# Kernel optimization log

Measured on AMD Instinct MI355X. Metric: run time of the kernel, lower is better.

The kernel has to match this reference:

```python
import jax, jax.numpy as jnp
import numpy as np

NUM_GRAPHS = 128

def gcn_conv(x, edge_index, W, b):
    # PyG GCNConv: add self-loops, sym-normalize, aggregate.
    n = x.shape[0]
    src, dst = edge_index[0], edge_index[1]
    h = x @ W                                   # [N, H]
    deg = jnp.zeros((n,), h.dtype).at[dst].add(1.0) + 1.0  # +1 for self-loop
    dinv = jax.lax.rsqrt(deg)                   # deg^-1/2
    norm = dinv[src] * dinv[dst]                # [E]
    msg = h[src] * norm[:, None]                # [E, H] gathered messages
    agg = jnp.zeros_like(h).at[dst].add(msg)    # scatter-add to dst
    agg = agg + h * (dinv * dinv)[:, None]      # self-loop term
    return agg + b


def setup_inputs() -> dict:
    key = jax.random.key(0)
    ks = jax.random.split(key, 12)
    N, E, F, H, C = 50000, 800000, 64, 64, 16
    x = jax.random.normal(ks[0], (N, F), jnp.float32)
    edge_index = jax.random.randint(ks[1], (2, E), 0, N, jnp.int64)
    batch = jnp.sort(jax.random.randint(ks[2], (N,), 0, NUM_GRAPHS, jnp.int64))
    s = lambda k, sh: jax.random.normal(k, sh, jnp.float32) * (1.0 / np.sqrt(sh[0]))
    return {
        "x": x, "edge_index": edge_index, "batch": batch,
        "W1": s(ks[3], (F, H)), "b1": jnp.zeros((H,), jnp.float32),
        "W2": s(ks[4], (H, H)), "b2": jnp.zeros((H,), jnp.float32),
        "Wc1": s(ks[5], (H, H)), "bc1": jnp.zeros((H,), jnp.float32),
        "Wc2": s(ks[6], (H, C)), "bc2": jnp.zeros((C,), jnp.float32),
    }


def reference(x, edge_index, batch, W1, b1, W2, b2, Wc1, bc1, Wc2, bc2):
    h = gcn_conv(x, edge_index, W1, b1)
    h = jax.nn.relu(h)
    # F.dropout(p=0.5, training=self.training): identity in eval mode
    h = gcn_conv(h, edge_index, W2, b2)
    # global mean pool over graphs
    sums = jax.ops.segment_sum(h, batch, num_segments=NUM_GRAPHS)
    cnts = jax.ops.segment_sum(jnp.ones((h.shape[0],), h.dtype), batch,
                               num_segments=NUM_GRAPHS)
    graph_reps = sums / jnp.maximum(cnts, 1.0)[:, None]
    logits = jax.nn.relu(graph_reps @ Wc1 + bc1) @ Wc2 + bc2
    return (h, graph_reps, logits)
```

## Files before the change

### kernel.cpp

```cpp
#include <hip/hip_runtime.h>
#include <hip/hip_bf16.h>

typedef __hip_bfloat16 bf16;

#define NGRAPH 128
#define MAXNB 256
#define BCAP 8192

__global__ __launch_bounds__(256) void bucket_count_kernel(const int* __restrict__ ei,
                                                           int* __restrict__ bucket_cnt,
                                                           int E, int N, int nb) {
    __shared__ int hist[MAXNB];
    for (int i = threadIdx.x; i < nb; i += 256) hist[i] = 0;
    __syncthreads();
    int stride = gridDim.x * 256;
    for (int e = blockIdx.x * 256 + threadIdx.x; e < E; e += stride) {
        int d = ei[E + e];
        d = max(0, min(d, N - 1));
        atomicAdd(&hist[d >> 8], 1);
    }
    __syncthreads();
    for (int i = threadIdx.x; i < nb; i += 256) {
        int c = hist[i];
        if (c) atomicAdd(&bucket_cnt[i], c);
    }
}

__global__ __launch_bounds__(256) void bucket_scan_kernel(const int* __restrict__ bucket_cnt,
                                                          int* __restrict__ bucket_off,
                                                          int* __restrict__ bucket_cur, int nb) {
    __shared__ int tmp[256];
    int tid = threadIdx.x;
    int v = (tid < nb) ? bucket_cnt[tid] : 0;
    tmp[tid] = v;
    __syncthreads();
    for (int off = 1; off < 256; off <<= 1) {
        int t = (tid >= off) ? tmp[tid - off] : 0;
        __syncthreads();
        tmp[tid] += t;
        __syncthreads();
    }
    int excl = tmp[tid] - v;
    if (tid < nb) { bucket_off[tid] = excl; bucket_cur[tid] = excl; }
    if (tid == nb - 1) bucket_off[nb] = excl + v;
}

__global__ __launch_bounds__(256) void bucket_scatter_kernel(const int* __restrict__ ei,
                                                             int* __restrict__ bucket_cur,
                                                             int* __restrict__ pairbuf,
                                                             int E, int N, int nb) {
    __shared__ int hist[MAXNB];
    int nwg = gridDim.x;
    int chunk = (E + nwg - 1) / nwg;
    int e0 = blockIdx.x * chunk;
    int e1 = e0 + chunk; if (e1 > E) e1 = E;
    if (e0 >= e1) return;
    for (int i = threadIdx.x; i < nb; i += 256) hist[i] = 0;
    __syncthreads();
    for (int e = e0 + threadIdx.x; e < e1; e += 256) {
        int d = ei[E + e];
        d = max(0, min(d, N - 1));
        atomicAdd(&hist[d >> 8], 1);
    }
    __syncthreads();
    for (int i = threadIdx.x; i < nb; i += 256) {
        int c = hist[i];
        hist[i] = c ? atomicAdd(&bucket_cur[i], c) : 0;
    }
    __syncthreads();
    for (int e = e0 + threadIdx.x; e < e1; e += 256) {
        int s = ei[e];     s = max(0, min(s, N - 1));
        int d = ei[E + e]; d = max(0, min(d, N - 1));
        int pos = atomicAdd(&hist[d >> 8], 1);
        pairbuf[pos] = (s << 8) | (d & 255);
    }
}

__global__ __launch_bounds__(256) void bucket_build_kernel(const int* __restrict__ pairbuf,
                                                           const int* __restrict__ bucket_off,
                                                           int* __restrict__ row_start,
                                                           float* __restrict__ dinv,
                                                           int* __restrict__ csr_src,
                                                           int E, int N, int nb) {
    __shared__ int deg_l[256];
    __shared__ int cur_l[256];
    __shared__ int stage[BCAP];
    int b = blockIdx.x;
    int node0 = b << 8;
    int nn = N - node0; if (nn > 256) nn = 256;
    int p0 = bucket_off[b], p1 = bucket_off[b + 1];
    int ne = p1 - p0;
    int tid = threadIdx.x;
    deg_l[tid] = 0;
    __syncthreads();
    for (int i = p0 + tid; i < p1; i += 256) {
        int dl = pairbuf[i] & 255;
        atomicAdd(&deg_l[dl], 1);
    }
    __syncthreads();
    int v = deg_l[tid];
    for (int off = 1; off < 256; off <<= 1) {
        int t = (tid >= off) ? deg_l[tid - off] : 0;
        __syncthreads();
        deg_l[tid] += t;
        __syncthreads();
    }
    int excl = deg_l[tid] - v;
    if (tid < nn) {
        row_start[node0 + tid] = p0 + excl;
        dinv[node0 + tid] = rsqrtf((float)(v + 1));
    }
    if (b == nb - 1 && tid == nn - 1) row_start[N] = p0 + excl + v;
    cur_l[tid] = excl;
    __syncthreads();
    if (ne <= BCAP) {
        for (int i = p0 + tid; i < p1; i += 256) {
            int pr = pairbuf[i];
            int pos = atomicAdd(&cur_l[pr & 255], 1);
            stage[pos] = pr >> 8;
        }
        __syncthreads();
        for (int i = tid; i < ne; i += 256) csr_src[p0 + i] = stage[i];
    } else {
        for (int i = p0 + tid; i < p1; i += 256) {
            int pr = pairbuf[i];
            int pos = atomicAdd(&cur_l[pr & 255], 1);
            csr_src[p0 + pos] = pr >> 8;
        }
    }
}

__global__ __launch_bounds__(256) void proj_kernel(const float* __restrict__ A,
                                                   const float* __restrict__ W,
                                                   const float* __restrict__ dinv,
                                                   bf16* __restrict__ P, int N) {
    __shared__ float Wl[4096];
    for (int i = threadIdx.x; i < 4096; i += 256) Wl[i] = W[i];
    __syncthreads();
    int lane = threadIdx.x & 63;
    int wid = (blockIdx.x * 256 + threadIdx.x) >> 6;
    int nwaves = (gridDim.x * 256) >> 6;
    for (int node = wid; node < N; node += nwaves) {
        float a = A[(size_t)node * 64 + lane];
        float acc = 0.f;
#pragma unroll
        for (int k = 0; k < 64; ++k) acc += __shfl(a, k) * Wl[k * 64 + lane];
        P[(size_t)node * 64 + lane] = __float2bfloat16(acc * dinv[node]);
    }
}

__device__ __forceinline__ void acc_bf8(float* acc, uint4 v, float w) {
    unsigned int u[4] = {v.x, v.y, v.z, v.w};
#pragma unroll
    for (int m = 0; m < 4; ++m) {
        float lo = __uint_as_float(u[m] << 16);
        float hi = __uint_as_float(u[m] & 0xffff0000u);
        acc[2 * m]     += w * lo;
        acc[2 * m + 1] += w * hi;
    }
}

__device__ __forceinline__ void gather_sum8(float* acc,
                                            const bf16* __restrict__ P,
                                            const int* __restrict__ csr_src,
                                            int beg, int end, int r, int c) {
#pragma unroll
    for (int k = 0; k < 8; ++k) acc[k] = 0.f;
    for (int i = beg; i < end; i += 16) {
        int r0 = i + r, r1 = i + 8 + r;
        int ok0 = (r0 < end), ok1 = (r1 < end);
        int s0 = ok0 ? csr_src[r0] : 0;
        int s1 = ok1 ? csr_src[r1] : 0;
        float w0 = ok0 ? 1.f : 0.f;
        float w1 = ok1 ? 1.f : 0.f;
        uint4 v0 = *(const uint4*)(P + (size_t)s0 * 64 + c * 8);
        uint4 v1 = *(const uint4*)(P + (size_t)s1 * 64 + c * 8);
        acc_bf8(acc, v0, w0);
        acc_bf8(acc, v1, w1);
    }
#pragma unroll
    for (int mask = 8; mask <= 32; mask <<= 1) {
#pragma unroll
        for (int k = 0; k < 8; ++k) acc[k] += __shfl_xor(acc[k], mask);
    }
}

__global__ __launch_bounds__(256) void agg_proj_kernel(const bf16* __restrict__ P1,
                                                       const int* __restrict__ row_start,
                                                       const int* __restrict__ csr_src,
                                                       const float* __restrict__ dinv,
                                                       const float* __restrict__ b1,
                                                       const float* __restrict__ W2,
                                                       bf16* __restrict__ P2, int N) {
    __shared__ float Wl[4096];
    for (int i = threadIdx.x; i < 4096; i += 256) Wl[i] = W2[i];
    __syncthreads();
    int lane = threadIdx.x & 63;
    int r = lane >> 3, c = lane & 7;
    float bb[8];
#pragma unroll
    for (int k = 0; k < 8; ++k) bb[k] = b1[c * 8 + k];
    int wid = (blockIdx.x * 256 + threadIdx.x) >> 6;
    int nwaves = (gridDim.x * 256) >> 6;
    int cpn = (N + nwaves - 1) / nwaves;
    int node0 = wid * cpn;
    int node1 = node0 + cpn; if (node1 > N) node1 = N;
    for (int node = node0; node < node1; ++node) {
        float acc[8];
        gather_sum8(acc, P1, csr_src, row_start[node], row_start[node + 1], r, c);
        uint4 vs = *(const uint4*)(P1 + (size_t)node * 64 + c * 8);
        acc_bf8(acc, vs, 1.f);
        float dv = dinv[node];
        float h[8];
#pragma unroll
        for (int k = 0; k < 8; ++k) h[k] = fmaxf(acc[k] * dv + bb[k], 0.f);
        float acc2 = 0.f;
#pragma unroll
        for (int c2 = 0; c2 < 8; ++c2) {
#pragma unroll
            for (int j = 0; j < 8; ++j) {
                acc2 += __shfl(h[j], c2) * Wl[(c2 * 8 + j) * 64 + lane];
            }
        }
        P2[(size_t)node * 64 + lane] = __float2bfloat16(acc2 * dv);
    }
}

__global__ __launch_bounds__(256) void agg_pool_kernel(const bf16* __restrict__ P2,
                                                       const int* __restrict__ row_start,
                                                       const int* __restrict__ csr_src,
                                                       const float* __restrict__ dinv,
                                                       const float* __restrict__ b2,
                                                       const int* __restrict__ batch,
                                                       float* __restrict__ out_h,
                                                       float* __restrict__ accum, int N) {
    int lane = threadIdx.x & 63;
    int r = lane >> 3, c = lane & 7;
    float bb[8];
#pragma unroll
    for (int k = 0; k < 8; ++k) bb[k] = b2[c * 8 + k];
    int src = ((lane & 7) << 3) | (lane >> 3);
    int wid = (blockIdx.x * 256 + threadIdx.x) >> 6;
    int nwaves = (gridDim.x * 256) >> 6;
    int cpn = (N + nwaves - 1) / nwaves;
    int node0 = wid * cpn;
    int node1 = node0 + cpn; if (node1 > N) node1 = N;
    for (int node = node0; node < node1; ++node) {
        float acc[8];
        gather_sum8(acc, P2, csr_src, row_start[node], row_start[node + 1], r, c);
        uint4 vs = *(const uint4*)(P2 + (size_t)node * 64 + c * 8);
        acc_bf8(acc, vs, 1.f);
        float dv = dinv[node];
        float h[8];
#pragma unroll
        for (int k = 0; k < 8; ++k) h[k] = acc[k] * dv + bb[k];
        float val = 0.f;
#pragma unroll
        for (int k = 0; k < 8; ++k) {
            float t = __shfl(h[k], src);
            val = ((lane & 7) == k) ? t : val;
        }
        out_h[(size_t)node * 64 + lane] = val;
        int g = batch[node];
        g = max(0, min(g, NGRAPH - 1));
        atomicAdd(&accum[g * 64 + lane], val);
    }
}

__device__ __forceinline__ int lower_bound_dev(const int* a, int n, int key) {
    int lo = 0, hi = n;
    while (lo < hi) {
        int mid = (lo + hi) >> 1;
        if (a[mid] < key) lo = mid + 1; else hi = mid;
    }
    return lo;
}

__global__ __launch_bounds__(64) void final_kernel(const float* __restrict__ accum,
                                                   const int* __restrict__ batch,
                                                   const float* __restrict__ Wc1,
                                                   const float* __restrict__ bc1,
                                                   const float* __restrict__ Wc2,
                                                   const float* __restrict__ bc2,
                                                   float* __restrict__ out_reps,
                                                   float* __restrict__ out_logits, int N) {
    __shared__ float rep[64];
    __shared__ float t[64];
    int g = blockIdx.x;
    int f = threadIdx.x;
    int lo = lower_bound_dev(batch, N, g);
    int hi = lower_bound_dev(batch, N, g + 1);
    float cnt = (float)(hi - lo);
    float r = accum[g * 64 + f] / fmaxf(cnt, 1.f);
    out_reps[g * 64 + f] = r;
    rep[f] = r;
    __syncthreads();
    float acc = bc1[f];
#pragma unroll
    for (int k = 0; k < 64; ++k) acc += rep[k] * Wc1[k * 64 + f];
    t[f] = fmaxf(acc, 0.f);
    __syncthreads();
    if (f < 16) {
        float a2 = bc2[f];
#pragma unroll
        for (int k = 0; k < 64; ++k) a2 += t[k] * Wc2[k * 16 + f];
        out_logits[g * 16 + f] = a2;
    }
}

extern "C" void kernel_launch(void* const* d_in, const int* in_sizes, int n_in,
                              void* d_out, int out_size, void* d_ws, size_t ws_size,
                              hipStream_t stream) {
    const float* x    = (const float*)d_in[0];
    const int*   ei   = (const int*)d_in[1];
    const int*   batch= (const int*)d_in[2];
    const float* W1   = (const float*)d_in[3];
    const float* b1   = (const float*)d_in[4];
    const float* W2   = (const float*)d_in[5];
    const float* b2   = (const float*)d_in[6];
    const float* Wc1  = (const float*)d_in[7];
    const float* bc1  = (const float*)d_in[8];
    const float* Wc2  = (const float*)d_in[9];
    const float* bc2  = (const float*)d_in[10];

    const int N = in_sizes[2];
    const int E = in_sizes[1] / 2;
    const int nb = (N + 255) >> 8;

    char* ws = (char*)d_ws;
    size_t off = 0;
    auto alloc = [&](size_t bytes) { void* p = ws + off; off += (bytes + 255) & ~(size_t)255; return p; };
    float* accum      = (float*)alloc((size_t)NGRAPH * 64 * 4);
    int*   bucket_cnt = (int*)  alloc((size_t)MAXNB * 4);
    size_t zero_bytes = off;
    int*   bucket_off = (int*)  alloc((size_t)(MAXNB + 1) * 4);
    int*   bucket_cur = (int*)  alloc((size_t)MAXNB * 4);
    float* dinv       = (float*)alloc((size_t)N * 4);
    int*   row_start  = (int*)  alloc((size_t)(N + 1) * 4);
    int*   csr_src    = (int*)  alloc((size_t)E * 4);
    bf16*  P1         = (bf16*) alloc((size_t)N * 64 * 2);
    size_t p2_bytes   = (size_t)N * 64 * 2;
    size_t pair_bytes = (size_t)E * 4;
    void*  p2_region  = alloc(p2_bytes > pair_bytes ? p2_bytes : pair_bytes);
    bf16*  P2         = (bf16*)p2_region;
    int*   pairbuf    = (int*)p2_region;
    (void)ws_size; (void)n_in; (void)out_size;

    float* out_h      = (float*)d_out;
    float* out_reps   = out_h + (size_t)N * 64;
    float* out_logits = out_reps + (size_t)NGRAPH * 64;

    const int GS = 2048;

    hipMemsetAsync(d_ws, 0, zero_bytes, stream);
    bucket_count_kernel<<<256, 256, 0, stream>>>(ei, bucket_cnt, E, N, nb);
    bucket_scan_kernel<<<1, 256, 0, stream>>>(bucket_cnt, bucket_off, bucket_cur, nb);
    bucket_scatter_kernel<<<256, 256, 0, stream>>>(ei, bucket_cur, pairbuf, E, N, nb);
    bucket_build_kernel<<<nb, 256, 0, stream>>>(pairbuf, bucket_off, row_start, dinv,
                                                csr_src, E, N, nb);

    proj_kernel<<<GS, 256, 0, stream>>>(x, W1, dinv, P1, N);
    agg_proj_kernel<<<GS, 256, 0, stream>>>(P1, row_start, csr_src, dinv, b1, W2, P2, N);
    agg_pool_kernel<<<GS, 256, 0, stream>>>(P2, row_start, csr_src, dinv, b2, batch,
                                            out_h, accum, N);
    final_kernel<<<NGRAPH, 64, 0, stream>>>(accum, batch, Wc1, bc1, Wc2, bc2,
                                            out_reps, out_logits, N);
}
```

Measured before the change: 250.2 us.

## Fuse first projection with bucket counting and fold scan into consumers

Runs the first-layer projection in the same launch as the destination bucket histogram, with separate block ranges for each job, so the projection no longer waits on dinv. The source-side dinv scaling moves into the layer-1 gather as a per-edge weight loaded from dinv[src]. The standalone bucket scan kernel is removed: the prefix sum is recomputed redundantly in the scatter and build kernels. This cuts two launches and a serialization point, but adds a dinv gather per edge and a repeated 256-element scan in every block.

New measurement: 247.2 us. Within noise of the previous version (-1.2%).

```diff
diff --git a/kernel.cpp b/kernel.cpp
--- a/kernel.cpp
+++ b/kernel.cpp
@@ -7,68 +7,81 @@
 #define MAXNB 256
 #define BCAP 8192
 
-__global__ __launch_bounds__(256) void bucket_count_kernel(const int* __restrict__ ei,
-                                                           int* __restrict__ bucket_cnt,
-                                                           int E, int N, int nb) {
+__global__ __launch_bounds__(256) void projB1_kernel(const int* __restrict__ ei,
+                                                     int* __restrict__ bucket_cnt,
+                                                     const float* __restrict__ A,
+                                                     const float* __restrict__ W,
+                                                     bf16* __restrict__ P,
+                                                     int E, int N, int nb) {
+    __shared__ float Wl[4096];
+    int* hist = (int*)Wl;
+    if ((int)blockIdx.x < 256) {
+        for (int i = threadIdx.x; i < nb; i += 256) hist[i] = 0;
+        __syncthreads();
+        int stride = 256 * 256;
+        for (int e = blockIdx.x * 256 + threadIdx.x; e < E; e += stride) {
+            int d = ei[E + e];
+            d = max(0, min(d, N - 1));
+            atomicAdd(&hist[d >> 8], 1);
+        }
+        __syncthreads();
+        for (int i = threadIdx.x; i < nb; i += 256) {
+            int c = hist[i];
+            if (c) atomicAdd(&bucket_cnt[i], c);
+        }
+        return;
+    }
+    for (int i = threadIdx.x; i < 4096; i += 256) Wl[i] = W[i];
+    __syncthreads();
+    int lane = threadIdx.x & 63;
+    int wid = (((int)blockIdx.x - 256) * 256 + threadIdx.x) >> 6;
+    int nwaves = (((int)gridDim.x - 256) * 256) >> 6;
+    for (int node = wid; node < N; node += nwaves) {
+        float a = A[(size_t)node * 64 + lane];
+        float acc = 0.f;
+#pragma unroll
+        for (int k = 0; k < 64; ++k) acc += __shfl(a, k) * Wl[k * 64 + lane];
+        P[(size_t)node * 64 + lane] = __float2bfloat16(acc);
+    }
+}
+
+__global__ __launch_bounds__(256) void bucket_scatter_kernel(const int* __restrict__ ei,
+                                                             const int* __restrict__ bucket_cnt,
+                                                             int* __restrict__ bucket_cur_rel,
+                                                             int* __restrict__ pairbuf,
+                                                             int E, int N, int nb) {
+    __shared__ int boff_l[MAXNB];
     __shared__ int hist[MAXNB];
-    for (int i = threadIdx.x; i < nb; i += 256) hist[i] = 0;
-    __syncthreads();
-    int stride = gridDim.x * 256;
-    for (int e = blockIdx.x * 256 + threadIdx.x; e < E; e += stride) {
-        int d = ei[E + e];
-        d = max(0, min(d, N - 1));
-        atomicAdd(&hist[d >> 8], 1);
-    }
-    __syncthreads();
-    for (int i = threadIdx.x; i < nb; i += 256) {
-        int c = hist[i];
-        if (c) atomicAdd(&bucket_cnt[i], c);
-    }
-}
-
-__global__ __launch_bounds__(256) void bucket_scan_kernel(const int* __restrict__ bucket_cnt,
-                                                          int* __restrict__ bucket_off,
-                                                          int* __restrict__ bucket_cur, int nb) {
-    __shared__ int tmp[256];
     int tid = threadIdx.x;
     int v = (tid < nb) ? bucket_cnt[tid] : 0;
-    tmp[tid] = v;
+    boff_l[tid] = v;
     __syncthreads();
     for (int off = 1; off < 256; off <<= 1) {
-        int t = (tid >= off) ? tmp[tid - off] : 0;
-        __syncthreads();
-        tmp[tid] += t;
-        __syncthreads();
-    }
-    int excl = tmp[tid] - v;
-    if (tid < nb) { bucket_off[tid] = excl; bucket_cur[tid] = excl; }
-    if (tid == nb - 1) bucket_off[nb] = excl + v;
-}
-
-__global__ __launch_bounds__(256) void bucket_scatter_kernel(const int* __restrict__ ei,
-                                                             int* __restrict__ bucket_cur,
-                                                             int* __restrict__ pairbuf,
-                                                             int E, int N, int nb) {
-    __shared__ int hist[MAXNB];
+        int t = (tid >= off) ? boff_l[tid - off] : 0;
+        __syncthreads();
+        boff_l[tid] += t;
+        __syncthreads();
+    }
+    boff_l[tid] -= v;
     int nwg = gridDim.x;
     int chunk = (E + nwg - 1) / nwg;
     int e0 = blockIdx.x * chunk;
     int e1 = e0 + chunk; if (e1 > E) e1 = E;
+    for (int i = tid; i < nb; i += 256) hist[i] = 0;
+    __syncthreads();
     if (e0 >= e1) return;
-    for (int i = threadIdx.x; i < nb; i += 256) hist[i] = 0;
-    __syncthreads();
-    for (int e = e0 + threadIdx.x; e < e1; e += 256) {
+    for (int e = e0 + tid; e < e1; e += 256) {
         int d = ei[E + e];
         d = max(0, min(d, N - 1));
         atomicAdd(&hist[d >> 8], 1);
     }
     __syncthreads();
-    for (int i = threadIdx.x; i < nb; i += 256) {
+    for (int i = tid; i < nb; i += 256) {
         int c = hist[i];
-        hist[i] = c ? atomicAdd(&bucket_cur[i], c) : 0;
-    }
-    __syncthreads();
-    for (int e = e0 + threadIdx.x; e < e1; e += 256) {
+        hist[i] = c ? (boff_l[i] + atomicAdd(&bucket_cur_rel[i], c)) : 0;
+    }
+    __syncthreads();
+    for (int e = e0 + tid; e < e1; e += 256) {
         int s = ei[e];     s = max(0, min(s, N - 1));
         int d = ei[E + e]; d = max(0, min(d, N - 1));
         int pos = atomicAdd(&hist[d >> 8], 1);
@@ -77,7 +90,7 @@
 }
 
 __global__ __launch_bounds__(256) void bucket_build_kernel(const int* __restrict__ pairbuf,
-                                                           const int* __restrict__ bucket_off,
+                                                           const int* __restrict__ bucket_cnt,
                                                            int* __restrict__ row_start,
                                                            float* __restrict__ dinv,
                                                            int* __restrict__ csr_src,
@@ -88,9 +101,20 @@
     int b = blockIdx.x;
     int node0 = b << 8;
     int nn = N - node0; if (nn > 256) nn = 256;
-    int p0 = bucket_off[b], p1 = bucket_off[b + 1];
+    int tid = threadIdx.x;
+    int cv = (tid < nb) ? bucket_cnt[tid] : 0;
+    cur_l[tid] = cv;
+    __syncthreads();
+    for (int off = 1; off < 256; off <<= 1) {
+        int t = (tid >= off) ? cur_l[tid - off] : 0;
+        __syncthreads();
+        cur_l[tid] += t;
+        __syncthreads();
+    }
+    int p1 = cur_l[b];
+    int p0 = p1 - ((b < nb) ? bucket_cnt[b] : 0);
     int ne = p1 - p0;
-    int tid = threadIdx.x;
+    __syncthreads();
     deg_l[tid] = 0;
     __syncthreads();
     for (int i = p0 + tid; i < p1; i += 256) {
@@ -110,7 +134,7 @@
         row_start[node0 + tid] = p0 + excl;
         dinv[node0 + tid] = rsqrtf((float)(v + 1));
     }
-    if (b == nb - 1 && tid == nn - 1) row_start[N] = p0 + excl + v;
+    if (b == nb - 1 && tid == 0) row_start[N] = p1;
     cur_l[tid] = excl;
     __syncthreads();
     if (ne <= BCAP) {
@@ -130,25 +154,6 @@
     }
 }
 
-__global__ __launch_bounds__(256) void proj_kernel(const float* __restrict__ A,
-                                                   const float* __restrict__ W,
-                                                   const float* __restrict__ dinv,
-                                                   bf16* __restrict__ P, int N) {
-    __shared__ float Wl[4096];
-    for (int i = threadIdx.x; i < 4096; i += 256) Wl[i] = W[i];
-    __syncthreads();
-    int lane = threadIdx.x & 63;
-    int wid = (blockIdx.x * 256 + threadIdx.x) >> 6;
-    int nwaves = (gridDim.x * 256) >> 6;
-    for (int node = wid; node < N; node += nwaves) {
-        float a = A[(size_t)node * 64 + lane];
-        float acc = 0.f;
-#pragma unroll
-        for (int k = 0; k < 64; ++k) acc += __shfl(a, k) * Wl[k * 64 + lane];
-        P[(size_t)node * 64 + lane] = __float2bfloat16(acc * dinv[node]);
-    }
-}
-
 __device__ __forceinline__ void acc_bf8(float* acc, uint4 v, float w) {
     unsigned int u[4] = {v.x, v.y, v.z, v.w};
 #pragma unroll
@@ -157,6 +162,32 @@
         float hi = __uint_as_float(u[m] & 0xffff0000u);
         acc[2 * m]     += w * lo;
         acc[2 * m + 1] += w * hi;
+    }
+}
+
+__device__ __forceinline__ void gather_sum8_w(float* acc,
+                                              const bf16* __restrict__ P,
+                                              const int* __restrict__ csr_src,
+                                              const float* __restrict__ dinv,
+                                              int beg, int end, int r, int c) {
+#pragma unroll
+    for (int k = 0; k < 8; ++k) acc[k] = 0.f;
+    for (int i = beg; i < end; i += 16) {
+        int r0 = i + r, r1 = i + 8 + r;
+        int ok0 = (r0 < end), ok1 = (r1 < end);
+        int s0 = ok0 ? csr_src[r0] : 0;
+        int s1 = ok1 ? csr_src[r1] : 0;
+        float w0 = ok0 ? dinv[s0] : 0.f;
+        float w1 = ok1 ? dinv[s1] : 0.f;
+        uint4 v0 = *(const uint4*)(P + (size_t)s0 * 64 + c * 8);
+        uint4 v1 = *(const uint4*)(P + (size_t)s1 * 64 + c * 8);
+        acc_bf8(acc, v0, w0);
+        acc_bf8(acc, v1, w1);
+    }
+#pragma unroll
+    for (int mask = 8; mask <= 32; mask <<= 1) {
+#pragma unroll
+        for (int k = 0; k < 8; ++k) acc[k] += __shfl_xor(acc[k], mask);
     }
 }
 
@@ -193,13 +224,12 @@
                                                        const float* __restrict__ W2,
                                                        bf16* __restrict__ P2, int N) {
     __shared__ float Wl[4096];
+    __shared__ float bl[64];
     for (int i = threadIdx.x; i < 4096; i += 256) Wl[i] = W2[i];
+    if (threadIdx.x < 64) bl[threadIdx.x] = b1[threadIdx.x];
     __syncthreads();
     int lane = threadIdx.x & 63;
     int r = lane >> 3, c = lane & 7;
-    float bb[8];
-#pragma unroll
-    for (int k = 0; k < 8; ++k) bb[k] = b1[c * 8 + k];
     int wid = (blockIdx.x * 256 + threadIdx.x) >> 6;
     int nwaves = (gridDim.x * 256) >> 6;
     int cpn = (N + nwaves - 1) / nwaves;
@@ -207,13 +237,13 @@
     int node1 = node0 + cpn; if (node1 > N) node1 = N;
     for (int node = node0; node < node1; ++node) {
         float acc[8];
-        gather_sum8(acc, P1, csr_src, row_start[node], row_start[node + 1], r, c);
+        gather_sum8_w(acc, P1, csr_src, dinv, row_start[node], row_start[node + 1], r, c);
+        float dv = dinv[node];
         uint4 vs = *(const uint4*)(P1 + (size_t)node * 64 + c * 8);
-        acc_bf8(acc, vs, 1.f);
-        float dv = dinv[node];
+        acc_bf8(acc, vs, dv);
         float h[8];
 #pragma unroll
-        for (int k = 0; k < 8; ++k) h[k] = fmaxf(acc[k] * dv + bb[k], 0.f);
+        for (int k = 0; k < 8; ++k) h[k] = fmaxf(acc[k] * dv + bl[c * 8 + k], 0.f);
         float acc2 = 0.f;
 #pragma unroll
         for (int c2 = 0; c2 < 8; ++c2) {
@@ -330,20 +360,19 @@
     char* ws = (char*)d_ws;
     size_t off = 0;
     auto alloc = [&](size_t bytes) { void* p = ws + off; off += (bytes + 255) & ~(size_t)255; return p; };
-    float* accum      = (float*)alloc((size_t)NGRAPH * 64 * 4);
-    int*   bucket_cnt = (int*)  alloc((size_t)MAXNB * 4);
-    size_t zero_bytes = off;
-    int*   bucket_off = (int*)  alloc((size_t)(MAXNB + 1) * 4);
-    int*   bucket_cur = (int*)  alloc((size_t)MAXNB * 4);
-    float* dinv       = (float*)alloc((size_t)N * 4);
-    int*   row_start  = (int*)  alloc((size_t)(N + 1) * 4);
-    int*   csr_src    = (int*)  alloc((size_t)E * 4);
-    bf16*  P1         = (bf16*) alloc((size_t)N * 64 * 2);
-    size_t p2_bytes   = (size_t)N * 64 * 2;
-    size_t pair_bytes = (size_t)E * 4;
-    void*  p2_region  = alloc(p2_bytes > pair_bytes ? p2_bytes : pair_bytes);
-    bf16*  P2         = (bf16*)p2_region;
-    int*   pairbuf    = (int*)p2_region;
+    float* accum       = (float*)alloc((size_t)NGRAPH * 64 * 4);
+    int*   bucket_cnt  = (int*)  alloc((size_t)MAXNB * 4);
+    int*   bucket_cur  = (int*)  alloc((size_t)MAXNB * 4);
+    size_t zero_bytes  = off;
+    float* dinv        = (float*)alloc((size_t)N * 4);
+    int*   row_start   = (int*)  alloc((size_t)(N + 1) * 4);
+    int*   csr_src     = (int*)  alloc((size_t)E * 4);
+    bf16*  P1          = (bf16*) alloc((size_t)N * 64 * 2);
+    size_t p2_bytes    = (size_t)N * 64 * 2;
+    size_t pair_bytes  = (size_t)E * 4;
+    void*  p2_region   = alloc(p2_bytes > pair_bytes ? p2_bytes : pair_bytes);
+    bf16*  P2          = (bf16*)p2_region;
+    int*   pairbuf     = (int*)p2_region;
     (void)ws_size; (void)n_in; (void)out_size;
 
     float* out_h      = (float*)d_out;
@@ -353,13 +382,12 @@
     const int GS = 2048;
 
     hipMemsetAsync(d_ws, 0, zero_bytes, stream);
-    bucket_count_kernel<<<256, 256, 0, stream>>>(ei, bucket_cnt, E, N, nb);
-    bucket_scan_kernel<<<1, 256, 0, stream>>>(bucket_cnt, bucket_off, bucket_cur, nb);
-    bucket_scatter_kernel<<<256, 256, 0, stream>>>(ei, bucket_cur, pairbuf, E, N, nb);
-    bucket_build_kernel<<<nb, 256, 0, stream>>>(pairbuf, bucket_off, row_start, dinv,
+    projB1_kernel<<<256 + GS, 256, 0, stream>>>(ei, bucket_cnt, x, W1, P1, E, N, nb);
+    bucket_scatter_kernel<<<256, 256, 0, stream>>>(ei, bucket_cnt, bucket_cur,
+                                                   pairbuf, E, N, nb);
+    bucket_build_kernel<<<nb, 256, 0, stream>>>(pairbuf, bucket_cnt, row_start, dinv,
                                                 csr_src, E, N, nb);
 
-    proj_kernel<<<GS, 256, 0, stream>>>(x, W1, dinv, P1, N);
     agg_proj_kernel<<<GS, 256, 0, stream>>>(P1, row_start, csr_src, dinv, b1, W2, P2, N);
     agg_pool_kernel<<<GS, 256, 0, stream>>>(P2, row_start, csr_src, dinv, b2, batch,
                                             out_h, accum, N);
```
